# Performance work log

Hardware: AMD Instinct MI355X
Metric: run time of the kernel (lower is better)

## Reference

```python
import jax, jax.numpy as jnp
import numpy as np

LAM = 1.0  # Lame lambda
MU = 1.0   # shear modulus
DT = 0.0


def energy_density(gradU, Q, dt):
    # compressible neo-Hookean strain energy density (per quad point)
    dim = gradU.shape[-1]
    F = gradU + jnp.eye(dim, dtype=gradU.dtype)
    J = jnp.linalg.det(F)
    logJ = jnp.log(J)
    I1 = jnp.sum(F * F)
    return 0.5 * MU * (I1 - dim) - MU * logJ + 0.5 * LAM * logJ * logJ


def lagrangian_density(Uq, gradU, Q, Xq, dt):
    # strain_energy_density_to_lagrangian_density: L ignores Uq and Xq
    return energy_density(gradU, Q, dt)


def integrate_element_from_local_field(elDisp, elCoords, elQ, dt, elShapes, elShapeGrads, elVols):
    # elDisp: [nn, d], elShapes: [nqp, nn], elShapeGrads: [nqp, nn, d], elVols: [nqp]
    gradU = jnp.einsum('ai,qaj->qij', elDisp, elShapeGrads)   # [nqp, d, d]
    Uq = jnp.einsum('qa,ai->qi', elShapes, elDisp)            # [nqp, d]
    Xq = jnp.einsum('qa,ai->qi', elShapes, elCoords)          # [nqp, d]
    Wq = jax.vmap(lagrangian_density, (0, 0, 0, 0, None))(Uq, gradU, elQ, Xq, dt)
    return jnp.sum(elVols * Wq)


def setup_inputs() -> dict:
    key = jax.random.key(0)
    kU, kC, kS, kG, kV, kQ = jax.random.split(key, 6)
    E, N, NN, D, Q = 250000, 64000, 4, 3, 1
    U = 0.01 * jax.random.normal(kU, (N, D), dtype=jnp.float32)  # small disp keeps det(F)>0
    coords = jax.random.uniform(kC, (N, D), dtype=jnp.float32)
    state = jax.random.normal(kQ, (E, Q, 1), dtype=jnp.float32)
    shapes = jax.random.uniform(kS, (E, Q, NN), dtype=jnp.float32)
    shape_grads = jax.random.normal(kG, (E, Q, NN, D), dtype=jnp.float32)
    vols = jax.random.uniform(kV, (E, Q), dtype=jnp.float32)
    conns = jax.random.randint(jax.random.fold_in(key, 7), (E, NN), 0, N, dtype=jnp.int32)
    return {"U": U, "coords": coords, "state": state, "shapes": shapes,
            "shape_grads": shape_grads, "vols": vols, "conns": conns}


def reference(U, coords, state, shapes, shape_grads, vols, conns):
    # compute_element_stiffnesses: per-element Hessian of integrated energy wrt elDisp
    def elem_stiff(elConn, elQ, elShapes, elShapeGrads, elVols):
        elDisp = U[elConn, :]      # gather via irregular connectivity
        elCoords = coords[elConn, :]
        return jax.hessian(integrate_element_from_local_field, argnums=0)(
            elDisp, elCoords, elQ, DT, elShapes, elShapeGrads, elVols)
    # output: [E, nn, d, nn, d]
    return jax.vmap(elem_stiff)(conns, state, shapes, shape_grads, vols)
```

## Files before the change

### kernel.cpp

```cpp
#include <hip/hip_runtime.h>
#include <math.h>


struct ElemData {
    float g[4][3];
    float dot[4][4];
    float c1, c2, c3;
};

__device__ __forceinline__ ElemData compute_elem(
    const float* __restrict__ U,
    const float* __restrict__ shape_grads,
    const float* __restrict__ vols,
    const int*  __restrict__ conns,
    size_t e)
{
    ElemData d;
    int4 cc = *reinterpret_cast<const int4*>(conns + e * 4);
    const float4* gp = reinterpret_cast<const float4*>(shape_grads + e * 12);
    float4 q0 = gp[0], q1 = gp[1], q2 = gp[2];
    float G[4][3];
    G[0][0]=q0.x; G[0][1]=q0.y; G[0][2]=q0.z;
    G[1][0]=q0.w; G[1][1]=q1.x; G[1][2]=q1.y;
    G[2][0]=q1.z; G[2][1]=q1.w; G[2][2]=q2.x;
    G[3][0]=q2.y; G[3][1]=q2.z; G[3][2]=q2.w;

    float vol = vols[e];

    float F[3][3] = {{1.f,0.f,0.f},{0.f,1.f,0.f},{0.f,0.f,1.f}};
    int ca[4] = {cc.x, cc.y, cc.z, cc.w};
    #pragma unroll
    for (int a = 0; a < 4; ++a) {
        float u0 = U[(size_t)ca[a]*3 + 0];
        float u1 = U[(size_t)ca[a]*3 + 1];
        float u2 = U[(size_t)ca[a]*3 + 2];
        #pragma unroll
        for (int j = 0; j < 3; ++j) {
            F[0][j] = fmaf(u0, G[a][j], F[0][j]);
            F[1][j] = fmaf(u1, G[a][j], F[1][j]);
            F[2][j] = fmaf(u2, G[a][j], F[2][j]);
        }
    }

    float c00 = F[1][1]*F[2][2] - F[1][2]*F[2][1];
    float c01 = F[1][2]*F[2][0] - F[1][0]*F[2][2];
    float c02 = F[1][0]*F[2][1] - F[1][1]*F[2][0];
    float det = F[0][0]*c00 + F[0][1]*c01 + F[0][2]*c02;
    float invdet = 1.0f / det;
    float logJ = logf(det);

    float Fi[3][3];
    Fi[0][0] = c00*invdet;
    Fi[1][0] = c01*invdet;
    Fi[2][0] = c02*invdet;
    Fi[0][1] = (F[0][2]*F[2][1]-F[0][1]*F[2][2])*invdet;
    Fi[1][1] = (F[0][0]*F[2][2]-F[0][2]*F[2][0])*invdet;
    Fi[2][1] = (F[0][1]*F[2][0]-F[0][0]*F[2][1])*invdet;
    Fi[0][2] = (F[0][1]*F[1][2]-F[0][2]*F[1][1])*invdet;
    Fi[1][2] = (F[0][2]*F[1][0]-F[0][0]*F[1][2])*invdet;
    Fi[2][2] = (F[0][0]*F[1][1]-F[0][1]*F[1][0])*invdet;

    #pragma unroll
    for (int a = 0; a < 4; ++a)
        #pragma unroll
        for (int i = 0; i < 3; ++i)
            d.g[a][i] = G[a][0]*Fi[0][i] + G[a][1]*Fi[1][i] + G[a][2]*Fi[2][i];

    #pragma unroll
    for (int a = 0; a < 4; ++a)
        #pragma unroll
        for (int b = 0; b < 4; ++b)
            d.dot[a][b] = G[a][0]*G[b][0] + G[a][1]*G[b][1] + G[a][2]*G[b][2];

    const float MUc = 1.0f, LAMc = 1.0f;
    d.c1 = vol * MUc;
    d.c2 = vol * LAMc;
    d.c3 = vol * (MUc - LAMc * logJ);
    return d;
}

__device__ __forceinline__ void make_row(const ElemData& d, int a, int i,
                                         float4& r0, float4& r1, float4& r2)
{
    float row[12];
    float gai = d.g[a][i];
    #pragma unroll
    for (int b = 0; b < 4; ++b) {
        #pragma unroll
        for (int k = 0; k < 3; ++k) {
            float v = d.c2 * gai * d.g[b][k] + d.c3 * d.g[a][k] * d.g[b][i];
            if (i == k) v = fmaf(d.c1, d.dot[a][b], v);
            row[b*3 + k] = v;
        }
    }
    r0 = make_float4(row[0], row[1], row[2],  row[3]);
    r1 = make_float4(row[4], row[5], row[6],  row[7]);
    r2 = make_float4(row[8], row[9], row[10], row[11]);
}

__device__ __forceinline__ void lds_fence() {
    __builtin_amdgcn_sched_barrier(0);
    __builtin_amdgcn_wave_barrier();
    __builtin_amdgcn_sched_barrier(0);
}

__global__ __launch_bounds__(256) void mech_hess_kernel(
    const float* __restrict__ U,
    const float* __restrict__ shape_grads,
    const float* __restrict__ vols,
    const int*  __restrict__ conns,
    float* __restrict__ out,
    int E)
{
    __shared__ float4 buf[4][16 * 37];

    int tid  = threadIdx.x;
    int wave = tid >> 6;
    int lane = tid & 63;
    size_t e = (size_t)blockIdx.x * 256 + tid;

    bool fullBlock = ((size_t)blockIdx.x * 256 + 256) <= (size_t)E;

    if (fullBlock) {
        ElemData d = compute_elem(U, shape_grads, vols, conns, e);
        float4* ob = reinterpret_cast<float4*>(out);

        #pragma unroll
        for (int c = 0; c < 4; ++c) {
            if ((lane >> 4) == c) {
                int m = lane & 15;
                float4* wb = &buf[wave][m * 37];
                #pragma unroll
                for (int a = 0; a < 4; ++a) {
                    #pragma unroll
                    for (int i = 0; i < 3; ++i) {
                        float4 r0, r1, r2;
                        make_row(d, a, i, r0, r1, r2);
                        int j = (a*3 + i) * 3;
                        wb[j+0] = r0; wb[j+1] = r1; wb[j+2] = r2;
                    }
                }
            }
            lds_fence();
            size_t chunkF4 = ((size_t)blockIdx.x * 256 + wave*64 + c*16) * 36;
            #pragma unroll
            for (int it = 0; it < 9; ++it) {
                int s = it*64 + lane;
                int elem = s / 36;
                int slot = s + elem;
                ob[chunkF4 + s] = buf[wave][slot];
            }
            lds_fence();
        }
    } else {
        if (e < (size_t)E) {
            ElemData d = compute_elem(U, shape_grads, vols, conns, e);
            float* o = out + e * 144;
            #pragma unroll
            for (int a = 0; a < 4; ++a) {
                #pragma unroll
                for (int i = 0; i < 3; ++i) {
                    float4 r0, r1, r2;
                    make_row(d, a, i, r0, r1, r2);
                    float4* op = reinterpret_cast<float4*>(o + a*36 + i*12);
                    op[0] = r0; op[1] = r1; op[2] = r2;
                }
            }
        }
    }
}

extern "C" void kernel_launch(void* const* d_in, const int* in_sizes, int n_in,
                              void* d_out, int out_size, void* d_ws, size_t ws_size,
                              hipStream_t stream) {
    const float* U           = (const float*)d_in[0];
    const float* shape_grads = (const float*)d_in[4];
    const float* vols        = (const float*)d_in[5];
    const int*   conns       = (const int*)d_in[6];
    float* out = (float*)d_out;

    int E = in_sizes[5];

    int block = 256;
    int grid = (E + block - 1) / block;
    mech_hess_kernel<<<grid, block, 0, stream>>>(U, shape_grads, vols, conns, out, E);
}
```

Before: 33.97 us.

## Spread Hessian row computation across all lanes via LDS-staged element data

Each 16-lane group now writes its compact per-element data (shape-gradient products, dot products, coefficients) to shared memory. Then all 64 lanes cooperate: every lane computes one node-row block (three rows) for one of 16 elements, instead of only 16 lanes computing all 12 rows while the other 48 idle. This removes the 4x divergence in the output-generation phase at the cost of an extra LDS round trip, a wave barrier and more shared memory per block. It also switches to ext_vector_type f4 for the stores.

```diff
diff --git a/kernel.cpp b/kernel.cpp
--- a/kernel.cpp
+++ b/kernel.cpp
@@ -1,6 +1,8 @@
 #include <hip/hip_runtime.h>
 #include <math.h>
 
+
+typedef float f4 __attribute__((ext_vector_type(4)));
 
 struct ElemData {
     float g[4][3];
@@ -16,7 +18,9 @@
     size_t e)
 {
     ElemData d;
-    int4 cc = *reinterpret_cast<const int4*>(conns + e * 4);
+    i4_alias:;
+    const int4* cp = reinterpret_cast<const int4*>(conns + e * 4);
+    int4 cc = *cp;
     const float4* gp = reinterpret_cast<const float4*>(shape_grads + e * 12);
     float4 q0 = gp[0], q1 = gp[1], q2 = gp[2];
     float G[4][3];
@@ -80,7 +84,7 @@
 }
 
 __device__ __forceinline__ void make_row(const ElemData& d, int a, int i,
-                                         float4& r0, float4& r1, float4& r2)
+                                         f4& r0, f4& r1, f4& r2)
 {
     float row[12];
     float gai = d.g[a][i];
@@ -93,9 +97,9 @@
             row[b*3 + k] = v;
         }
     }
-    r0 = make_float4(row[0], row[1], row[2],  row[3]);
-    r1 = make_float4(row[4], row[5], row[6],  row[7]);
-    r2 = make_float4(row[8], row[9], row[10], row[11]);
+    r0 = (f4){row[0], row[1], row[2],  row[3]};
+    r1 = (f4){row[4], row[5], row[6],  row[7]};
+    r2 = (f4){row[8], row[9], row[10], row[11]};
 }
 
 __device__ __forceinline__ void lds_fence() {
@@ -112,7 +116,8 @@
     float* __restrict__ out,
     int E)
 {
-    __shared__ float4 buf[4][16 * 37];
+    __shared__ float edata[4][16 * 36];
+    __shared__ f4    buf[4][16 * 37];
 
     int tid  = threadIdx.x;
     int wave = tid >> 6;
@@ -123,22 +128,57 @@
 
     if (fullBlock) {
         ElemData d = compute_elem(U, shape_grads, vols, conns, e);
-        float4* ob = reinterpret_cast<float4*>(out);
+        f4* ob = reinterpret_cast<f4*>(out);
 
         #pragma unroll
         for (int c = 0; c < 4; ++c) {
             if ((lane >> 4) == c) {
                 int m = lane & 15;
-                float4* wb = &buf[wave][m * 37];
+                float* ed = &edata[wave][m * 36];
+                f4 w0 = (f4){d.g[0][0], d.g[0][1], d.g[0][2], d.g[1][0]};
+                f4 w1 = (f4){d.g[1][1], d.g[1][2], d.g[2][0], d.g[2][1]};
+                f4 w2 = (f4){d.g[2][2], d.g[3][0], d.g[3][1], d.g[3][2]};
+                *reinterpret_cast<f4*>(ed + 0) = w0;
+                *reinterpret_cast<f4*>(ed + 4) = w1;
+                *reinterpret_cast<f4*>(ed + 8) = w2;
                 #pragma unroll
                 for (int a = 0; a < 4; ++a) {
+                    f4 wd = (f4){d.dot[a][0], d.dot[a][1], d.dot[a][2], d.dot[a][3]};
+                    *reinterpret_cast<f4*>(ed + 12 + 4*a) = wd;
+                }
+                f4 wc = (f4){d.c1, d.c2, d.c3, 0.f};
+                *reinterpret_cast<f4*>(ed + 28) = wc;
+            }
+            lds_fence();
+            {
+                int el2 = lane >> 2;
+                int r   = lane & 3;
+                const float* ed = &edata[wave][el2 * 36];
+                f4 ga = *reinterpret_cast<const f4*>(ed + 0);
+                f4 gb = *reinterpret_cast<const f4*>(ed + 4);
+                f4 gc = *reinterpret_cast<const f4*>(ed + 8);
+                f4 dr = *reinterpret_cast<const f4*>(ed + 12 + 4*r);
+                f4 cv = *reinterpret_cast<const f4*>(ed + 28);
+                float g[12] = {ga[0],ga[1],ga[2],ga[3],gb[0],gb[1],gb[2],gb[3],
+                               gc[0],gc[1],gc[2],gc[3]};
+                float c1 = cv[0], c2 = cv[1], c3 = cv[2];
+                f4* wb = &buf[wave][el2 * 37 + r * 9];
+                #pragma unroll
+                for (int i = 0; i < 3; ++i) {
+                    float gai = g[r*3 + i];
+                    float row[12];
                     #pragma unroll
-                    for (int i = 0; i < 3; ++i) {
-                        float4 r0, r1, r2;
-                        make_row(d, a, i, r0, r1, r2);
-                        int j = (a*3 + i) * 3;
-                        wb[j+0] = r0; wb[j+1] = r1; wb[j+2] = r2;
+                    for (int b = 0; b < 4; ++b) {
+                        #pragma unroll
+                        for (int k = 0; k < 3; ++k) {
+                            float v = c2 * gai * g[b*3 + k] + c3 * g[r*3 + k] * g[b*3 + i];
+                            if (i == k) v = fmaf(c1, dr[b], v);
+                            row[b*3 + k] = v;
+                        }
                     }
+                    wb[i*3 + 0] = (f4){row[0], row[1], row[2],  row[3]};
+                    wb[i*3 + 1] = (f4){row[4], row[5], row[6],  row[7]};
+                    wb[i*3 + 2] = (f4){row[8], row[9], row[10], row[11]};
                 }
             }
             lds_fence();
@@ -155,15 +195,16 @@
     } else {
         if (e < (size_t)E) {
             ElemData d = compute_elem(U, shape_grads, vols, conns, e);
-            float* o = out + e * 144;
+            f4* o = reinterpret_cast<f4*>(out + e * 144);
             #pragma unroll
             for (int a = 0; a < 4; ++a) {
                 #pragma unroll
                 for (int i = 0; i < 3; ++i) {
-                    float4 r0, r1, r2;
+                    f4 r0, r1, r2;
                     make_row(d, a, i, r0, r1, r2);
-                    float4* op = reinterpret_cast<float4*>(o + a*36 + i*12);
-                    op[0] = r0; op[1] = r1; op[2] = r2;
+                    o[(a*3+i)*3 + 0] = r0;
+                    o[(a*3+i)*3 + 1] = r1;
+                    o[(a*3+i)*3 + 2] = r2;
                 }
             }
         }
```

Measured after the change: 33.72 us. About the same (-0.7%).
